# Kernel tuning notes

Hardware: AMD Instinct MI355X
Metric: run time of the kernel (lower is better)

The kernel has to match this reference:

```python
import jax, jax.numpy as jnp
import numpy as np
import math

NUM_HEADS = 8
MAX_BIAS = 8.0


def _alibi_slopes(n):
    def p2(m):
        start = 2.0 ** (-(2.0 ** (-(math.log2(m) - 3.0))))
        return [start * (start ** i) for i in range(m)]
    if math.log2(n).is_integer():
        return p2(n)
    c = 2 ** int(math.floor(math.log2(n)))
    return p2(c) + _alibi_slopes(2 * c)[0::2][: n - c]


def _rope_sin_cos(N, D, dtype):
    # freqs: [N, D/2]; sin/cos tiled twice along last dim -> [N, D] (NeoX style)
    inv = 1.0 / (10000.0 ** (jnp.arange(0, D, 2, dtype=jnp.float32) / D))
    f = jnp.arange(N, dtype=jnp.float32)[:, None] * inv[None, :]
    sin = jnp.concatenate([jnp.sin(f), jnp.sin(f)], axis=-1)
    cos = jnp.concatenate([jnp.cos(f), jnp.cos(f)], axis=-1)
    return sin.astype(dtype), cos.astype(dtype)


def _rotate_half(x):
    x1, x2 = jnp.split(x, 2, axis=-1)
    return jnp.concatenate([-x2, x1], axis=-1)


def setup_inputs() -> dict:
    key = jax.random.key(0)
    k1, k2, k3 = jax.random.split(key, 3)
    B, N, C = 4, 2048, 512
    x = jax.random.normal(k1, (B, N, C), jnp.float32)
    qkv_w = jax.random.normal(k2, (3 * C, C), jnp.float32) * (C ** -0.5)
    proj_w = jax.random.normal(k3, (C, C), jnp.float32) * (C ** -0.5)
    proj_b = jnp.zeros((C,), jnp.float32)
    return {"x": x, "qkv_w": qkv_w, "proj_w": proj_w, "proj_b": proj_b}


def reference(x, qkv_w, proj_w, proj_b):
    B, N, C = x.shape
    H = NUM_HEADS
    D = C // H
    scale = D ** -0.5
    # qkv projection -> q,k,v each [B,H,N,D]
    qkv = (x @ qkv_w.T).reshape(B, N, 3, H, D).transpose(2, 0, 3, 1, 4)
    q, k, v = qkv[0], qkv[1], qkv[2]
    # inline RoPE on q and k
    sin, cos = _rope_sin_cos(N, D, x.dtype)  # [N, D]
    q = q * cos + _rotate_half(q) * sin
    k = k * cos + _rotate_half(k) * sin
    # full NxN scores
    attn = jnp.einsum('bhqd,bhkd->bhqk', q, k) * scale
    # ALiBi bias: slope per head, nonpositive relative distances
    pos = jnp.arange(N, dtype=jnp.float32)
    rel = jnp.minimum(pos[None, :] - pos[:, None], 0.0)  # [N, N]
    slopes = jnp.asarray(_alibi_slopes(H), dtype=jnp.float32)  # [H]
    alibi = rel[None, None, :, :] * slopes[None, :, None, None] * MAX_BIAS
    attn = attn + alibi.astype(attn.dtype)
    attn = jax.nn.softmax(attn, axis=-1)
    out = jnp.einsum('bhqk,bhkd->bhqd', attn, v)
    out = out.transpose(0, 2, 1, 3).reshape(B, N, C)
    return out @ proj_w.T + proj_b
```

## Files before the change

### kernel.cpp

```cpp
#include <hip/hip_runtime.h>

typedef unsigned short u16;
typedef unsigned int u32;
typedef __attribute__((ext_vector_type(8))) __bf16 bf16x8;
typedef __attribute__((ext_vector_type(4))) float f32x4;
typedef __attribute__((ext_vector_type(16))) float f32x16;
typedef __attribute__((ext_vector_type(4))) u16 u16x4;
typedef __attribute__((ext_vector_type(4))) u32 u32x4;

#define LOG2E 1.44269504088896f

__device__ __forceinline__ u16 f2bf(float f) {
  unsigned u = __builtin_bit_cast(unsigned, f);
  u += 0x7fffu + ((u >> 16) & 1u);
  return (u16)(u >> 16);
}
__device__ __forceinline__ float bf2f(u16 h) {
  unsigned u = ((unsigned)h) << 16;
  return __builtin_bit_cast(float, u);
}
__device__ __forceinline__ void gload16(void* lds, const void* g) {
  __builtin_amdgcn_global_load_lds(
      (const __attribute__((address_space(1))) void*)g,
      (__attribute__((address_space(3))) void*)lds, 16, 0, 0);
}
__device__ __forceinline__ f32x4 mfma16(bf16x8 a, bf16x8 b, f32x4 c) {
  return __builtin_amdgcn_mfma_f32_16x16x32_bf16(a, b, c, 0, 0, 0);
}
__device__ __forceinline__ f32x16 mfma32(bf16x8 a, bf16x8 b, f32x16 c) {
  return __builtin_amdgcn_mfma_f32_32x32x16_bf16(a, b, c, 0, 0, 0);
}
__device__ __forceinline__ float nexp2(float x) { return __builtin_amdgcn_exp2f(x); }
__device__ __forceinline__ float nrcp(float x) { return __builtin_amdgcn_rcpf(x); }

__device__ __constant__ unsigned char LB_TBL[128] = {
    0x00,0x10,0x40,0x41,0x70,0x71,0x72,0x73,0x74,0x75,0x76,0x77,0x78,0x79,0x7A,
    0x01,0x11,0x42,0x7B,0x02,0x12,0x43,0x7C,0x03,0x13,0x44,0x7D,0x04,0x14,0x45,
    0x7E,0x05,0x15,0x46,0x7F,0x06,0x16,0x47,0x07,0x17,0x48,0x08,0x18,0x49,0x09,
    0x19,0x4A,0x0A,0x1A,0x4B,0x0B,0x1B,0x4C,0x0C,0x1C,0x4D,0x0D,0x1D,0x4E,0x0E,
    0x1E,0x4F,0x0F,0x1F,
    0x20,0x30,0x31,0x50,0x51,0x52,0x53,0x60,0x61,0x62,0x63,0x64,0x65,
    0x21,0x32,0x54,0x66,0x22,0x33,0x55,0x67,0x23,0x34,0x56,0x68,0x24,0x35,0x57,
    0x69,0x25,0x36,0x58,0x6A,0x26,0x37,0x59,0x6B,0x27,0x38,0x5A,0x6C,0x28,0x39,
    0x5B,0x6D,0x29,0x3A,0x5C,0x6E,0x2A,0x3B,0x5D,0x6F,0x2B,0x3C,0x5E,0x2C,0x3D,
    0x5F,0x2D,0x3E,0x2E,0x3F,0x2F};

__global__ __launch_bounds__(256) void prep_kernel(const float* __restrict__ x,
                                                   const float* __restrict__ qkv_w,
                                                   const float* __restrict__ proj_w,
                                                   u16* __restrict__ XB,
                                                   u16* __restrict__ WQB,
                                                   u16* __restrict__ WPB,
                                                   float* __restrict__ sc) {
  const int bid = blockIdx.x, t = threadIdx.x;
  if (bid < 5120) {
    const float* src;
    u16* dst;
    size_t base;
    if (bid < 4096) { src = x; dst = XB; base = (size_t)bid; }
    else if (bid < 4864) { src = qkv_w; dst = WQB; base = (size_t)(bid - 4096); }
    else { src = proj_w; dst = WPB; base = (size_t)(bid - 4864); }
    size_t i = base * 256 + t;
    f32x4 v = *(const f32x4*)(src + i * 4);
    u16x4 o;
#pragma unroll
    for (int j = 0; j < 4; ++j) o[j] = f2bf(v[j]);
    *(u16x4*)(dst + i * 4) = o;
  } else {
    int i = (bid - 5120) * 256 + t;
    int n = i >> 5, d = i & 31;
    float inv = powf(10000.0f, -(float)d * (1.0f / 32.0f));
    float f = (float)n * inv;
    sc[(size_t)n * 64 + d] = sinf(f);
    sc[(size_t)n * 64 + 32 + d] = cosf(f);
  }
}

template <int MODE>
__global__ __launch_bounds__(256) void gemm_bt(const u16* __restrict__ A,
                                               const u16* __restrict__ Bw,
                                               float* __restrict__ Cout,
                                               const float* __restrict__ bias,
                                               const float* __restrict__ SC,
                                               u16* __restrict__ Qo,
                                               u16* __restrict__ Ko,
                                               u16* __restrict__ Vo,
                                               int M, int Nout, int K) {
  __shared__ u16 lA[2][128 * 32];
  __shared__ u16 lB[2][128 * 32];
  const int t = threadIdx.x;
  const int l = t & 63, w = t >> 6;
  const int lrow = l & 15, lg = l >> 4;
  constexpr int NB = (MODE == 2) ? 12 : 4;
  const int id = blockIdx.x;
  const int xcd = id & 7, kk = id >> 3;
  const int m0 = ((kk / NB) * 8 + xcd) * 128;
  const int n0 = (kk % NB) * 128;
  const int wr = (w >> 1) * 64, wc = (w & 1) * 64;
  f32x4 acc[4][4];
#pragma unroll
  for (int i = 0; i < 4; ++i)
#pragma unroll
    for (int j = 0; j < 4; ++j)
#pragma unroll
      for (int r = 0; r < 4; ++r) acc[i][j][r] = 0.f;

  const int srow = t >> 2;
  const int scb = (t & 3) * 16;
  const int nk = K >> 5;

  auto stageg = [&](int buf, int kt) {
#pragma unroll
    for (int c = 0; c < 2; ++c) {
      int row = c * 64 + srow;
      const char* ga = (const char*)A + ((size_t)(m0 + row) * K + kt * 32) * 2 + scb;
      const char* gb = (const char*)Bw + ((size_t)(n0 + row) * K + kt * 32) * 2 + scb;
      gload16((char*)&lA[buf][0] + c * 4096 + t * 16, ga);
      gload16((char*)&lB[buf][0] + c * 4096 + t * 16, gb);
    }
  };

  stageg(0, 0);
  __syncthreads();
  int cb = 0;
  for (int kt = 0; kt < nk; ++kt) {
    if (kt + 1 < nk) stageg(cb ^ 1, kt + 1);
    bf16x8 af[4], bfr[4];
#pragma unroll
    for (int i = 0; i < 4; ++i) {
      af[i] = *(const bf16x8*)((const char*)&lA[cb][0] + (wr + i * 16 + lrow) * 64 + lg * 16);
      bfr[i] = *(const bf16x8*)((const char*)&lB[cb][0] + (wc + i * 16 + lrow) * 64 + lg * 16);
    }
#pragma unroll
    for (int i = 0; i < 4; ++i)
#pragma unroll
      for (int j = 0; j < 4; ++j)
        acc[i][j] = mfma16(af[i], bfr[j], acc[i][j]);
    __syncthreads();
    cb ^= 1;
  }

  if constexpr (MODE == 0) {
#pragma unroll
    for (int i = 0; i < 4; ++i)
#pragma unroll
      for (int j = 0; j < 4; ++j)
#pragma unroll
        for (int r = 0; r < 4; ++r) {
          int m = m0 + wr + i * 16 + lg * 4 + r;
          int n = n0 + wc + j * 16 + lrow;
          Cout[(size_t)m * Nout + n] = acc[i][j][r] + bias[n];
        }
  } else {
    const int part = n0 >> 9;
    if (part < 2) {
      u16* Dst = (part == 0) ? Qo : Ko;
      const int hh = ((n0 & 511) + wc) >> 6;
#pragma unroll
      for (int i = 0; i < 4; ++i) {
#pragma unroll
        for (int r = 0; r < 4; ++r) {
          int m = m0 + wr + i * 16 + lg * 4 + r;
          int bb = m >> 11, nseq = m & 2047;
          const float* scrow = SC + (size_t)nseq * 64;
          u16* orow = Dst + ((size_t)(bb * 8 + hh) * 2048 + nseq) * 64;
#pragma unroll
          for (int j = 0; j < 2; ++j) {
            int dlo = j * 16 + lrow;
            float s = scrow[dlo], c = scrow[32 + dlo];
            float v1 = acc[i][j][r], v2 = acc[i][j + 2][r];
            orow[dlo] = f2bf(v1 * c - v2 * s);
            orow[dlo + 32] = f2bf(v2 * c + v1 * s);
          }
        }
      }
    } else {
#pragma unroll
      for (int i = 0; i < 4; ++i) {
        int m = m0 + wr + i * 16 + lg * 4;
        int bb = m >> 11, nseq = m & 2047;
#pragma unroll
        for (int j = 0; j < 4; ++j) {
          int pc = (n0 & 511) + wc + j * 16 + lrow;
          int hh = pc >> 6, d = pc & 63;
          u16x4 pk;
#pragma unroll
          for (int r = 0; r < 4; ++r) pk[r] = f2bf(acc[i][j][r]);
          *(u16x4*)(Vo + ((size_t)((bb * 8 + hh) * 64 + d)) * 2048 + nseq) = pk;
        }
      }
    }
  }
}

__global__ __launch_bounds__(512, 4) void attn_kernel(const u16* __restrict__ Q,
                                                      const u16* __restrict__ Kn,
                                                      const u16* __restrict__ Vt,
                                                      u16* __restrict__ Ob) {
  __shared__ u16 KV[2][2][2][4096];
  const int t = threadIdx.x, l = t & 63, w = t >> 6;
  const int li = l & 31, hi = l >> 5;
  const int half = w >> 2, g = w & 3;

  const int id = blockIdx.x + 32 * blockIdx.y;
  const int xcd = id & 7, slot = id >> 3;
  const int rank = slot < 32 ? slot : 95 - slot;
  const int item = LB_TBL[(xcd & 1) * 64 + rank];
  const int h = item >> 4, qt = item & 15;
  const int bh = (xcd >> 1) * 8 + h;
  const int b = xcd >> 1;

  const int qg = qt * 128 + g * 32 + li;
  const float sl2 = nexp2((float)(2 - h)) * LOG2E;
  const float sc2 = 0.125f * LOG2E;
  const int swz = (li & 7) << 4;

  const int wint = (int)(10.3974f * (float)(1 << h));
  int lo_i = 128 * qt + 64 - wint;
  const int lo = lo_i <= 0 ? 0 : (lo_i & ~63);
  const int T = (2048 - lo) >> 6;
  const int nIter = (T + 1) >> 1;

  bf16x8 qa[4];
  {
    const char* qb = (const char*)Q + ((size_t)bh * 2048 + qg) * 128 + hi * 16;
#pragma unroll
    for (int s = 0; s < 4; ++s) qa[s] = *(const bf16x8*)(qb + s * 32);
  }
  float cst[4];
#pragma unroll
  for (int j = 0; j < 4; ++j) cst[j] = (float)j * sl2;
  const float c8 = 8.f * sl2, c32 = 32.f * sl2;
  float vbm = (float)(4 * hi - qg) * sl2;
  float negm = 0.f;
  float lrun = 0.f;
  f32x16 oacc0, oacc1;
#pragma unroll
  for (int r = 0; r < 16; ++r) { oacc0[r] = 0.f; oacc1[r] = 0.f; }

  auto stage = [&](int buf, int it) {
#pragma unroll
    for (int c = 0; c < 4; ++c) {
      int o = c * 512 + t;
      int half_s = o >> 10, rem = o & 1023;
      int kv = rem >> 9, idx = rem & 511;
      int row = idx >> 3;
      int sb = ((idx & 7) * 16) ^ ((row & 7) << 4);
      int k0s = lo + (half_s ? nIter + it : it) * 64;
      if (k0s < 2048) {
        char* dst = (char*)KV + buf * 32768 + half_s * 16384 + kv * 8192 + idx * 16;
        const char* src;
        if (kv == 0)
          src = (const char*)Kn + ((size_t)(bh * 2048 + k0s + row)) * 128 + sb;
        else
          src = (const char*)Vt + ((size_t)(bh * 64 + row)) * 4096 +
                (size_t)k0s * 2 + sb;
        gload16(dst, src);
      }
    }
  };

  stage(0, 0);
  __syncthreads();
  int cur = 0;
  const char* myK = (const char*)KV + half * 16384;
  const char* myV = myK + 8192;
  for (int it = 0; it < nIter; ++it) {
    if (it + 1 < nIter) stage(cur ^ 1, it + 1);

    const int k0g = lo + (half ? nIter + it : it) * 64;
    const bool active = (k0g < 2048);
    if (active) {
      const float basem0 = fmaf((float)k0g, sl2, vbm);

      float ls0 = 0.f, ls1 = 0.f;
      bf16x8 pf[4];
#pragma unroll
      for (int kb = 0; kb < 2; ++kb) {
        f32x16 sa;
#pragma unroll
        for (int r = 0; r < 16; ++r) sa[r] = 0.f;
        const char* kb_base = myK + cur * 32768 + kb * 4096 + li * 128;
        __builtin_amdgcn_s_setprio(1);
#pragma unroll
        for (int s = 0; s < 4; ++s) {
          bf16x8 kf = *(const bf16x8*)(kb_base + ((s * 32 + hi * 16) ^ swz));
          sa = mfma32(kf, qa[s], sa);
        }
        __builtin_amdgcn_s_setprio(0);
        float bq[4];
        bq[0] = kb ? basem0 + c32 : basem0;
        bq[1] = bq[0] + c8;
        bq[2] = bq[1] + c8;
        bq[3] = bq[2] + c8;
        float p[16];
#pragma unroll
        for (int r = 0; r < 16; ++r)
          p[r] = fmaf(sa[r], sc2, fminf(bq[r >> 2] + cst[r & 3], negm));
#pragma unroll
        for (int r = 0; r < 16; r += 2) {
          float e0 = nexp2(p[r]), e1 = nexp2(p[r + 1]);
          p[r] = e0;
          p[r + 1] = e1;
          ls0 += e0;
          ls1 += e1;
        }
#pragma unroll
        for (int s = 0; s < 2; ++s) {
          u32 a0, b0, a1, b1;
          asm("v_cvt_pk_bf16_f32 %0, %1, %2" : "=v"(a0) : "v"(p[s * 8 + 0]), "v"(p[s * 8 + 1]));
          asm("v_cvt_pk_bf16_f32 %0, %1, %2" : "=v"(b0) : "v"(p[s * 8 + 4]), "v"(p[s * 8 + 5]));
          asm("v_cvt_pk_bf16_f32 %0, %1, %2" : "=v"(a1) : "v"(p[s * 8 + 2]), "v"(p[s * 8 + 3]));
          asm("v_cvt_pk_bf16_f32 %0, %1, %2" : "=v"(b1) : "v"(p[s * 8 + 6]), "v"(p[s * 8 + 7]));
          asm("v_permlane32_swap_b32 %0, %1" : "+v"(a0), "+v"(b0));
          asm("v_permlane32_swap_b32 %0, %1" : "+v"(a1), "+v"(b1));
          u32x4 fr;
          fr[0] = a0; fr[1] = a1; fr[2] = b0; fr[3] = b1;
          pf[kb * 2 + s] = __builtin_bit_cast(bf16x8, fr);
        }
      }
      float ls = ls0 + ls1;
      ls += __shfl_xor(ls, 32);
      lrun += ls;

      const char* vb_base = myV + cur * 32768 + li * 128;
      __builtin_amdgcn_s_setprio(1);
#pragma unroll
      for (int ks = 0; ks < 4; ++ks) {
        int off = (ks * 32 + hi * 16) ^ swz;
        bf16x8 vf0 = *(const bf16x8*)(vb_base + off);
        bf16x8 vf1 = *(const bf16x8*)(vb_base + 4096 + off);
        oacc0 = mfma32(vf0, pf[ks], oacc0);
        oacc1 = mfma32(vf1, pf[ks], oacc1);
      }
      __builtin_amdgcn_s_setprio(0);

      if (__any(lrun > 1e28f)) {
        vbm -= 64.f;
        negm -= 64.f;
        lrun *= 0x1p-64f;
#pragma unroll
        for (int r = 0; r < 16; ++r) {
          oacc0[r] *= 0x1p-64f;
          oacc1[r] *= 0x1p-64f;
        }
      }
    }
    __syncthreads();
    cur ^= 1;
  }

  float* S = (float*)KV;
  if (half == 1) {
    float* base = S + (size_t)g * 34 * 64;
#pragma unroll
    for (int r = 0; r < 16; ++r) {
      base[r * 64 + l] = oacc0[r];
      base[(16 + r) * 64 + l] = oacc1[r];
    }
    base[32 * 64 + l] = lrun;
    base[33 * 64 + l] = negm;
  }
  __syncthreads();
  if (half == 0) {
    const float* base = S + (size_t)g * 34 * 64;
    float lB = base[32 * 64 + l];
    float negmB = base[33 * 64 + l];
    float mA = -negm, mB = -negmB;
    float mS = fmaxf(mA, mB);
    float aA = nexp2(mA - mS), aB = nexp2(mB - mS);
    float linv = nrcp(fmaf(lrun, aA, lB * aB));
    float cA = aA * linv, cB = aB * linv;
    u16* orow = Ob + ((size_t)b * 2048 + qg) * 512 + h * 64;
#pragma unroll
    for (int db = 0; db < 2; ++db) {
#pragma unroll
      for (int gg = 0; gg < 4; ++gg) {
        u16x4 pk;
#pragma unroll
        for (int j = 0; j < 4; ++j) {
          int r = gg * 4 + j;
          float oA = db ? oacc1[r] : oacc0[r];
          float oB = base[(db * 16 + r) * 64 + l];
          pk[j] = f2bf(oA * cA + oB * cB);
        }
        *(u16x4*)(orow + db * 32 + gg * 8 + 4 * hi) = pk;
      }
    }
  }
}

extern "C" void kernel_launch(void* const* d_in, const int* in_sizes, int n_in,
                              void* d_out, int out_size, void* d_ws, size_t ws_size,
                              hipStream_t stream) {
  const float* x = (const float*)d_in[0];
  const float* qkv_w = (const float*)d_in[1];
  const float* proj_w = (const float*)d_in[2];
  const float* proj_b = (const float*)d_in[3];
  char* ws = (char*)d_ws;

  u16* XB = (u16*)(ws + 0);
  u16* WQB = (u16*)(ws + 8388608);
  u16* WPB = (u16*)(ws + 9961472);
  u16* QB = (u16*)(ws + 10485760);
  u16* KB = (u16*)(ws + 18874368);
  u16* VTB = (u16*)(ws + 27262976);
  u16* OB = (u16*)(ws + 35651584);
  float* SC = (float*)(ws + 44040192);

  prep_kernel<<<5376, 256, 0, stream>>>(x, qkv_w, proj_w, XB, WQB, WPB, SC);
  gemm_bt<2><<<768, 256, 0, stream>>>(XB, WQB, nullptr, nullptr, SC, QB,
                                      KB, VTB, 8192, 1536, 512);
  attn_kernel<<<dim3(32, 16), 512, 0, stream>>>(QB, KB, VTB, OB);
  gemm_bt<0><<<256, 256, 0, stream>>>(OB, WPB, (float*)d_out, proj_b,
                                      nullptr, nullptr, nullptr, nullptr,
                                      8192, 512, 512);
}
```

Measured before the change: 87.26 us.

## Specialize ALiBi bias per tile and drop running-max rescale in attention

Splits the per-tile score bias into three cases: tiles entirely above the diagonal skip the bias, tiles fully below skip the min clamp, and only diagonal-straddling tiles use the clamped form. It also removes the overflow guard that rescaled the accumulators (the shared negm offset), so the two half-merges become a simple sum, and it precomputes the staging source pointers so each iteration only adds a fixed step. This is meant to trim VALU work in the softmax inner loop and the address math in the staging loop. The risk is overflow: scores are now exponentiated without any max subtraction, which depends on scores staying bounded for these inputs.

```diff
diff --git a/kernel.cpp b/kernel.cpp
--- a/kernel.cpp
+++ b/kernel.cpp
@@ -210,7 +210,8 @@
   const int bh = (xcd >> 1) * 8 + h;
   const int b = xcd >> 1;
 
-  const int qg = qt * 128 + g * 32 + li;
+  const int qw0 = qt * 128 + g * 32;
+  const int qg = qw0 + li;
   const float sl2 = nexp2((float)(2 - h)) * LOG2E;
   const float sc2 = 0.125f * LOG2E;
   const int swz = (li & 7) << 4;
@@ -231,47 +232,55 @@
 #pragma unroll
   for (int j = 0; j < 4; ++j) cst[j] = (float)j * sl2;
   const float c8 = 8.f * sl2, c32 = 32.f * sl2;
-  float vbm = (float)(4 * hi - qg) * sl2;
-  float negm = 0.f;
+  const float vbm = (float)(4 * hi - qg) * sl2;
   float lrun = 0.f;
   f32x16 oacc0, oacc1;
 #pragma unroll
   for (int r = 0; r < 16; ++r) { oacc0[r] = 0.f; oacc1[r] = 0.f; }
 
-  auto stage = [&](int buf, int it) {
-#pragma unroll
-    for (int c = 0; c < 4; ++c) {
-      int o = c * 512 + t;
-      int half_s = o >> 10, rem = o & 1023;
-      int kv = rem >> 9, idx = rem & 511;
-      int row = idx >> 3;
-      int sb = ((idx & 7) * 16) ^ ((row & 7) << 4);
-      int k0s = lo + (half_s ? nIter + it : it) * 64;
-      if (k0s < 2048) {
-        char* dst = (char*)KV + buf * 32768 + half_s * 16384 + kv * 8192 + idx * 16;
-        const char* src;
-        if (kv == 0)
-          src = (const char*)Kn + ((size_t)(bh * 2048 + k0s + row)) * 128 + sb;
-        else
-          src = (const char*)Vt + ((size_t)(bh * 64 + row)) * 4096 +
-                (size_t)k0s * 2 + sb;
-        gload16(dst, src);
-      }
-    }
+  const char* sp[4];
+  int doff[4], k0c[4], step[4];
+#pragma unroll
+  for (int c = 0; c < 4; ++c) {
+    int o = c * 512 + t;
+    int half_s = o >> 10, rem = o & 1023;
+    int kv = rem >> 9, idx = rem & 511;
+    int row = idx >> 3;
+    int sb = ((idx & 7) * 16) ^ ((row & 7) << 4);
+    k0c[c] = lo + (half_s ? nIter : 0) * 64;
+    doff[c] = half_s * 16384 + kv * 8192 + idx * 16;
+    if (kv == 0) {
+      sp[c] = (const char*)Kn + ((size_t)(bh * 2048 + k0c[c] + row)) * 128 + sb;
+      step[c] = 8192;
+    } else {
+      sp[c] = (const char*)Vt + ((size_t)(bh * 64 + row)) * 4096 +
+              (size_t)k0c[c] * 2 + sb;
+      step[c] = 128;
+    }
+  }
+  auto stage_issue = [&](int buf) {
+#pragma unroll
+    for (int c = 0; c < 4; ++c)
+      if (k0c[c] < 2048) gload16((char*)KV + buf * 32768 + doff[c], sp[c]);
   };
-
-  stage(0, 0);
+  auto stage_adv = [&]() {
+#pragma unroll
+    for (int c = 0; c < 4; ++c) { sp[c] += step[c]; k0c[c] += 64; }
+  };
+
+  stage_issue(0);
+  stage_adv();
   __syncthreads();
   int cur = 0;
+  int k0g = lo + half * nIter * 64;
   const char* myK = (const char*)KV + half * 16384;
   const char* myV = myK + 8192;
   for (int it = 0; it < nIter; ++it) {
-    if (it + 1 < nIter) stage(cur ^ 1, it + 1);
-
-    const int k0g = lo + (half ? nIter + it : it) * 64;
-    const bool active = (k0g < 2048);
-    if (active) {
+    if (it + 1 < nIter) { stage_issue(cur ^ 1); stage_adv(); }
+
+    if (k0g < 2048) {
       const float basem0 = fmaf((float)k0g, sl2, vbm);
+      const int rel = k0g - qw0;
 
       float ls0 = 0.f, ls1 = 0.f;
       bf16x8 pf[4];
@@ -288,15 +297,27 @@
           sa = mfma32(kf, qa[s], sa);
         }
         __builtin_amdgcn_s_setprio(0);
-        float bq[4];
-        bq[0] = kb ? basem0 + c32 : basem0;
-        bq[1] = bq[0] + c8;
-        bq[2] = bq[1] + c8;
-        bq[3] = bq[2] + c8;
+        const int relk = rel + kb * 32;
         float p[16];
-#pragma unroll
-        for (int r = 0; r < 16; ++r)
-          p[r] = fmaf(sa[r], sc2, fminf(bq[r >> 2] + cst[r & 3], negm));
+        if (relk > 31) {
+#pragma unroll
+          for (int r = 0; r < 16; ++r) p[r] = sa[r] * sc2;
+        } else {
+          float bq[4];
+          bq[0] = kb ? basem0 + c32 : basem0;
+          bq[1] = bq[0] + c8;
+          bq[2] = bq[1] + c8;
+          bq[3] = bq[2] + c8;
+          if (relk < -63) {
+#pragma unroll
+            for (int r = 0; r < 16; ++r)
+              p[r] = fmaf(sa[r], sc2, bq[r >> 2] + cst[r & 3]);
+          } else {
+#pragma unroll
+            for (int r = 0; r < 16; ++r)
+              p[r] = fmaf(sa[r], sc2, fminf(bq[r >> 2] + cst[r & 3], 0.f));
+          }
+        }
 #pragma unroll
         for (int r = 0; r < 16; r += 2) {
           float e0 = nexp2(p[r]), e1 = nexp2(p[r + 1]);
@@ -334,43 +355,27 @@
         oacc1 = mfma32(vf1, pf[ks], oacc1);
       }
       __builtin_amdgcn_s_setprio(0);
-
-      if (__any(lrun > 1e28f)) {
-        vbm -= 64.f;
-        negm -= 64.f;
-        lrun *= 0x1p-64f;
-#pragma unroll
-        for (int r = 0; r < 16; ++r) {
-          oacc0[r] *= 0x1p-64f;
-          oacc1[r] *= 0x1p-64f;
-        }
-      }
     }
     __syncthreads();
     cur ^= 1;
+    k0g += 64;
   }
 
   float* S = (float*)KV;
   if (half == 1) {
-    float* base = S + (size_t)g * 34 * 64;
+    float* base = S + (size_t)g * 33 * 64;
 #pragma unroll
     for (int r = 0; r < 16; ++r) {
       base[r * 64 + l] = oacc0[r];
       base[(16 + r) * 64 + l] = oacc1[r];
     }
     base[32 * 64 + l] = lrun;
-    base[33 * 64 + l] = negm;
   }
   __syncthreads();
   if (half == 0) {
-    const float* base = S + (size_t)g * 34 * 64;
+    const float* base = S + (size_t)g * 33 * 64;
     float lB = base[32 * 64 + l];
-    float negmB = base[33 * 64 + l];
-    float mA = -negm, mB = -negmB;
-    float mS = fmaxf(mA, mB);
-    float aA = nexp2(mA - mS), aB = nexp2(mB - mS);
-    float linv = nrcp(fmaf(lrun, aA, lB * aB));
-    float cA = aA * linv, cB = aB * linv;
+    float linv = nrcp(lrun + lB);
     u16* orow = Ob + ((size_t)b * 2048 + qg) * 512 + h * 64;
 #pragma unroll
     for (int db = 0; db < 2; ++db) {
@@ -382,7 +387,7 @@
           int r = gg * 4 + j;
           float oA = db ? oacc1[r] : oacc0[r];
           float oB = base[(db * 16 + r) * 64 + l];
-          pk[j] = f2bf(oA * cA + oB * cB);
+          pk[j] = f2bf((oA + oB) * linv);
         }
         *(u16x4*)(orow + db * 32 + gg * 8 + 4 * hi) = pk;
       }
```

After: 115.3 us. 32.2% more time.

## Fuse fp32-to-bf16 input conversion into QKV GEMM tile loads

Applied to the files above, without the earlier changes.

The prep kernel no longer converts x to bf16. The QKV GEMM now stages fp32 x tiles into a larger, XOR-swizzled LDS buffer and converts them to bf16 in registers with v_cvt_pk_bf16_f32 just before the MFMA. This removes a full write and re-read of the bf16 copy of x, at the cost of doubling A-tile LDS traffic and adding conversion ALU work inside the GEMM loop. Separately, the RoPE epilogue now writes each rotated pair as one packed 2-element store in an interleaved head-dim layout. That permutation is applied to both Q and K, so their dot products are unchanged.

```diff
diff --git a/kernel.cpp b/kernel.cpp
--- a/kernel.cpp
+++ b/kernel.cpp
@@ -5,6 +5,7 @@
 typedef __attribute__((ext_vector_type(8))) __bf16 bf16x8;
 typedef __attribute__((ext_vector_type(4))) float f32x4;
 typedef __attribute__((ext_vector_type(16))) float f32x16;
+typedef __attribute__((ext_vector_type(2))) u16 u16x2;
 typedef __attribute__((ext_vector_type(4))) u16 u16x4;
 typedef __attribute__((ext_vector_type(4))) u32 u32x4;
 
@@ -45,21 +46,18 @@
     0x5B,0x6D,0x29,0x3A,0x5C,0x6E,0x2A,0x3B,0x5D,0x6F,0x2B,0x3C,0x5E,0x2C,0x3D,
     0x5F,0x2D,0x3E,0x2E,0x3F,0x2F};
 
-__global__ __launch_bounds__(256) void prep_kernel(const float* __restrict__ x,
-                                                   const float* __restrict__ qkv_w,
+__global__ __launch_bounds__(256) void prep_kernel(const float* __restrict__ qkv_w,
                                                    const float* __restrict__ proj_w,
-                                                   u16* __restrict__ XB,
                                                    u16* __restrict__ WQB,
                                                    u16* __restrict__ WPB,
                                                    float* __restrict__ sc) {
   const int bid = blockIdx.x, t = threadIdx.x;
-  if (bid < 5120) {
+  if (bid < 1024) {
     const float* src;
     u16* dst;
     size_t base;
-    if (bid < 4096) { src = x; dst = XB; base = (size_t)bid; }
-    else if (bid < 4864) { src = qkv_w; dst = WQB; base = (size_t)(bid - 4096); }
-    else { src = proj_w; dst = WPB; base = (size_t)(bid - 4864); }
+    if (bid < 768) { src = qkv_w; dst = WQB; base = (size_t)bid; }
+    else { src = proj_w; dst = WPB; base = (size_t)(bid - 768); }
     size_t i = base * 256 + t;
     f32x4 v = *(const f32x4*)(src + i * 4);
     u16x4 o;
@@ -67,7 +65,7 @@
     for (int j = 0; j < 4; ++j) o[j] = f2bf(v[j]);
     *(u16x4*)(dst + i * 4) = o;
   } else {
-    int i = (bid - 5120) * 256 + t;
+    int i = (bid - 1024) * 256 + t;
     int n = i >> 5, d = i & 31;
     float inv = powf(10000.0f, -(float)d * (1.0f / 32.0f));
     float f = (float)n * inv;
@@ -78,6 +76,7 @@
 
 template <int MODE>
 __global__ __launch_bounds__(256) void gemm_bt(const u16* __restrict__ A,
+                                               const float* __restrict__ Af,
                                                const u16* __restrict__ Bw,
                                                float* __restrict__ Cout,
                                                const float* __restrict__ bias,
@@ -86,7 +85,7 @@
                                                u16* __restrict__ Ko,
                                                u16* __restrict__ Vo,
                                                int M, int Nout, int K) {
-  __shared__ u16 lA[2][128 * 32];
+  __shared__ u16 lA[2][128 * ((MODE == 2) ? 64 : 32)];
   __shared__ u16 lB[2][128 * 32];
   const int t = threadIdx.x;
   const int l = t & 63, w = t >> 6;
@@ -110,12 +109,29 @@
   const int nk = K >> 5;
 
   auto stageg = [&](int buf, int kt) {
+    if constexpr (MODE == 2) {
+#pragma unroll
+      for (int c = 0; c < 4; ++c) {
+        int o = c * 256 + t;
+        int row = o >> 3;
+        int sb = ((o & 7) * 16) ^ ((row & 7) << 4);
+        const char* ga =
+            (const char*)Af + ((size_t)(m0 + row) * K + kt * 32) * 4 + sb;
+        gload16((char*)&lA[buf][0] + o * 16, ga);
+      }
+    } else {
+#pragma unroll
+      for (int c = 0; c < 2; ++c) {
+        int row = c * 64 + srow;
+        const char* ga =
+            (const char*)A + ((size_t)(m0 + row) * K + kt * 32) * 2 + scb;
+        gload16((char*)&lA[buf][0] + c * 4096 + t * 16, ga);
+      }
+    }
 #pragma unroll
     for (int c = 0; c < 2; ++c) {
       int row = c * 64 + srow;
-      const char* ga = (const char*)A + ((size_t)(m0 + row) * K + kt * 32) * 2 + scb;
       const char* gb = (const char*)Bw + ((size_t)(n0 + row) * K + kt * 32) * 2 + scb;
-      gload16((char*)&lA[buf][0] + c * 4096 + t * 16, ga);
       gload16((char*)&lB[buf][0] + c * 4096 + t * 16, gb);
     }
   };
@@ -128,7 +144,24 @@
     bf16x8 af[4], bfr[4];
 #pragma unroll
     for (int i = 0; i < 4; ++i) {
-      af[i] = *(const bf16x8*)((const char*)&lA[cb][0] + (wr + i * 16 + lrow) * 64 + lg * 16);
+      if constexpr (MODE == 2) {
+        int arow = wr + i * 16 + lrow;
+        int swzr = (arow & 7) << 4;
+        const char* ab = (const char*)&lA[cb][0] + arow * 128;
+        f32x4 alo = *(const f32x4*)(ab + ((lg * 32) ^ swzr));
+        f32x4 ahi = *(const f32x4*)(ab + ((lg * 32 + 16) ^ swzr));
+        u32 w0, w1, w2, w3;
+        asm("v_cvt_pk_bf16_f32 %0, %1, %2" : "=v"(w0) : "v"(alo[0]), "v"(alo[1]));
+        asm("v_cvt_pk_bf16_f32 %0, %1, %2" : "=v"(w1) : "v"(alo[2]), "v"(alo[3]));
+        asm("v_cvt_pk_bf16_f32 %0, %1, %2" : "=v"(w2) : "v"(ahi[0]), "v"(ahi[1]));
+        asm("v_cvt_pk_bf16_f32 %0, %1, %2" : "=v"(w3) : "v"(ahi[2]), "v"(ahi[3]));
+        u32x4 fr;
+        fr[0] = w0; fr[1] = w1; fr[2] = w2; fr[3] = w3;
+        af[i] = __builtin_bit_cast(bf16x8, fr);
+      } else {
+        af[i] = *(const bf16x8*)((const char*)&lA[cb][0] +
+                                 (wr + i * 16 + lrow) * 64 + lg * 16);
+      }
       bfr[i] = *(const bf16x8*)((const char*)&lB[cb][0] + (wc + i * 16 + lrow) * 64 + lg * 16);
     }
 #pragma unroll
@@ -169,8 +202,10 @@
             int dlo = j * 16 + lrow;
             float s = scrow[dlo], c = scrow[32 + dlo];
             float v1 = acc[i][j][r], v2 = acc[i][j + 2][r];
-            orow[dlo] = f2bf(v1 * c - v2 * s);
-            orow[dlo + 32] = f2bf(v2 * c + v1 * s);
+            u16x2 pr;
+            pr[0] = f2bf(v1 * c - v2 * s);
+            pr[1] = f2bf(v2 * c + v1 * s);
+            *(u16x2*)(orow + 2 * dlo) = pr;
           }
         }
       }
@@ -399,20 +434,19 @@
   const float* proj_b = (const float*)d_in[3];
   char* ws = (char*)d_ws;
 
-  u16* XB = (u16*)(ws + 0);
-  u16* WQB = (u16*)(ws + 8388608);
-  u16* WPB = (u16*)(ws + 9961472);
-  u16* QB = (u16*)(ws + 10485760);
-  u16* KB = (u16*)(ws + 18874368);
-  u16* VTB = (u16*)(ws + 27262976);
-  u16* OB = (u16*)(ws + 35651584);
-  float* SC = (float*)(ws + 44040192);
-
-  prep_kernel<<<5376, 256, 0, stream>>>(x, qkv_w, proj_w, XB, WQB, WPB, SC);
-  gemm_bt<2><<<768, 256, 0, stream>>>(XB, WQB, nullptr, nullptr, SC, QB,
+  u16* WQB = (u16*)(ws + 0);
+  u16* WPB = (u16*)(ws + 1572864);
+  u16* QB = (u16*)(ws + 2097152);
+  u16* KB = (u16*)(ws + 10485760);
+  u16* VTB = (u16*)(ws + 18874368);
+  u16* OB = (u16*)(ws + 27262976);
+  float* SC = (float*)(ws + 35651584);
+
+  prep_kernel<<<1280, 256, 0, stream>>>(qkv_w, proj_w, WQB, WPB, SC);
+  gemm_bt<2><<<768, 256, 0, stream>>>(nullptr, x, WQB, nullptr, nullptr, SC, QB,
                                       KB, VTB, 8192, 1536, 512);
   attn_kernel<<<dim3(32, 16), 512, 0, stream>>>(QB, KB, VTB, OB);
-  gemm_bt<0><<<256, 256, 0, stream>>>(OB, WPB, (float*)d_out, proj_b,
+  gemm_bt<0><<<256, 256, 0, stream>>>(OB, nullptr, WPB, (float*)d_out, proj_b,
                                       nullptr, nullptr, nullptr, nullptr,
                                       8192, 512, 512);
 }
```

New measurement: 97.69 us. 1.12x slower.
